# Optimization experiments

Hardware: AMD Instinct MI355X
Metric: run time of the kernel (lower is better)

The kernel has to match this reference:

```python
import jax, jax.numpy as jnp
import numpy as np

INPUT_DIMS = [300, 74, 35]
HIDDEN_DIMS = [512, 256, 256]
OUT_CELL = 256
OUT_DIM = 7
B, T = 128, 256


def setup_inputs() -> dict:
    key = jax.random.key(0)
    ks = jax.random.split(key, 32)
    inp = {}
    for i, d in enumerate(INPUT_DIMS):
        inp[f"x{i}"] = jax.random.normal(ks[i], (B, T, d), dtype=jnp.float32)
    ki = 3
    for i, (d, h) in enumerate(zip(INPUT_DIMS, HIDDEN_DIMS)):
        s_ih = 1.0 / np.sqrt(h)
        inp[f"W_ih{i}"] = jax.random.uniform(ks[ki + 0], (4 * h, d), jnp.float32, -s_ih, s_ih)
        inp[f"W_hh{i}"] = jax.random.uniform(ks[ki + 1], (4 * h, h), jnp.float32, -s_ih, s_ih)
        inp[f"b_ih{i}"] = jax.random.uniform(ks[ki + 2], (4 * h,), jnp.float32, -s_ih, s_ih)
        inp[f"b_hh{i}"] = jax.random.uniform(ks[ki + 3], (4 * h,), jnp.float32, -s_ih, s_ih)
        ki += 4
    H = sum(HIDDEN_DIMS)
    s1 = 1.0 / np.sqrt(H)
    s2 = 1.0 / np.sqrt(OUT_CELL)
    inp["fc_W1"] = jax.random.uniform(ks[ki + 0], (OUT_CELL, H), jnp.float32, -s1, s1)
    inp["fc_b1"] = jax.random.uniform(ks[ki + 1], (OUT_CELL,), jnp.float32, -s1, s1)
    inp["fc_W2"] = jax.random.uniform(ks[ki + 2], (OUT_DIM, OUT_CELL), jnp.float32, -s2, s2)
    inp["fc_b2"] = jax.random.uniform(ks[ki + 3], (OUT_DIM,), jnp.float32, -s2, s2)
    return inp


def _run_lstm(x, W_ih, W_hh, b_ih, b_hh):
    # x: [B, T, d] -> hidden trajectory [B, T, h]; PyTorch LSTMCell gate order i,f,g,o
    Bsz = x.shape[0]
    h4 = W_hh.shape[0]
    h = h4 // 4
    gx = jnp.einsum('btd,gd->btg', x, W_ih) + b_ih + b_hh  # precompute input contribution

    def step(carry, g_t):
        hp, cp = carry
        g = g_t + hp @ W_hh.T  # [B, 4h]
        i, f, gg, o = jnp.split(g, 4, axis=-1)
        c = jax.nn.sigmoid(f) * cp + jax.nn.sigmoid(i) * jnp.tanh(gg)
        hn = jax.nn.sigmoid(o) * jnp.tanh(c)
        return (hn, c), hn

    h0 = jnp.zeros((Bsz, h), x.dtype)
    c0 = jnp.zeros((Bsz, h), x.dtype)
    _, hs = jax.lax.scan(step, (h0, c0), gx.transpose(1, 0, 2))  # hs: [T, B, h]
    return hs.transpose(1, 0, 2)


def reference(x0, x1, x2,
              W_ih0, W_hh0, b_ih0, b_hh0,
              W_ih1, W_hh1, b_ih1, b_hh1,
              W_ih2, W_hh2, b_ih2, b_hh2,
              fc_W1, fc_b1, fc_W2, fc_b2):
    hs = [
        _run_lstm(x0, W_ih0, W_hh0, b_ih0, b_hh0),
        _run_lstm(x1, W_ih1, W_hh1, b_ih1, b_hh1),
        _run_lstm(x2, W_ih2, W_hh2, b_ih2, b_hh2),
    ]
    hcat = jnp.concatenate(hs, axis=-1)  # [B, T, sum(h)]
    # SimpleNet head (dropout identity at inference): Linear -> ReLU -> Linear
    z = jax.nn.relu(jnp.einsum('bth,ch->btc', hcat, fc_W1) + fc_b1)
    logits = jnp.einsum('btc,oc->bto', z, fc_W2) + fc_b2  # [B, T, out]
    return jax.nn.log_softmax(logits, axis=-1)
```

## Files before the change

kernel.cpp:

```cpp
#include <hip/hip_runtime.h>
#include <hip/hip_bf16.h>
#include <math.h>

typedef __hip_bfloat16 bf16;
typedef unsigned short ushort_t;
typedef unsigned long long ull_t;
typedef __attribute__((ext_vector_type(8))) short short8;
typedef __attribute__((ext_vector_type(4))) float f32x4;

constexpr int NB = 128;
constexpr int NT = 256;
constexpr int HCAT = 1024;
constexpr int KP0 = 320;
constexpr int KP1 = 128;
constexpr int KP2 = 64;

__device__ inline float bf2f(ushort_t u) {
  union { unsigned i; float f; } x; x.i = (unsigned)u << 16; return x.f;
}
__device__ inline ushort_t f2bf(float f) {
  bf16 b = __float2bfloat16(f);
  return *reinterpret_cast<ushort_t*>(&b);
}
__device__ inline float fsig(float x) {
  return __builtin_amdgcn_rcpf(1.f + __expf(-x));
}
__device__ inline float ftanh(float x) {
  return 2.f * __builtin_amdgcn_rcpf(1.f + __expf(-2.f * x)) - 1.f;
}

__global__ __launch_bounds__(256) void k_cvt_w(
    const float* __restrict__ in, ushort_t* __restrict__ out, int R, int K, int KP)
{
  int i = blockIdx.x * 256 + threadIdx.x;
  if (i >= R * KP) return;
  int r = i / KP, k = i - r * KP;
  out[i] = (k < K) ? f2bf(in[(size_t)r * K + k]) : (ushort_t)0;
}

__global__ __launch_bounds__(256) void k_cvt_x(
    const float* __restrict__ x, ushort_t* __restrict__ out,
    int d, int KP, int t0, int tcShift, int total)
{
  int i = blockIdx.x * 256 + threadIdx.x;
  if (i >= total) return;
  int row = i / KP, k = i - row * KP;
  int b = row >> tcShift, tl = row & ((1 << tcShift) - 1);
  out[i] = (k < d) ? f2bf(x[((size_t)b * NT + t0 + tl) * d + k]) : (ushort_t)0;
}

__global__ __launch_bounds__(256) void k_gemm(
    const ushort_t* __restrict__ A, const ushort_t* __restrict__ B, int KP,
    const float* __restrict__ bias0, const float* __restrict__ bias1,
    ushort_t* __restrict__ outb, float* __restrict__ outf, int ldc, int mode)
{
  __shared__ ushort_t As[2][64][72];
  __shared__ ushort_t Bs[2][64][72];
  const int row0 = blockIdx.x * 64;
  const int col0 = blockIdx.y * 64;
  const int tid  = threadIdx.x;
  const int lane = tid & 63;
  const int w    = tid >> 6;
  const int n    = lane & 15;
  const int quad = lane >> 4;
  const int sr = tid >> 2;
  const int sc = (tid & 3) * 16;

  const ushort_t* arow = A + (size_t)(row0 + sr) * KP + sc;
  const ushort_t* brow = B + (size_t)(col0 + sr) * KP + sc;

  short8 ra0 = *reinterpret_cast<const short8*>(arow);
  short8 ra1 = *reinterpret_cast<const short8*>(arow + 8);
  short8 rb0 = *reinterpret_cast<const short8*>(brow);
  short8 rb1 = *reinterpret_cast<const short8*>(brow + 8);
  *reinterpret_cast<short8*>(&As[0][sr][sc])     = ra0;
  *reinterpret_cast<short8*>(&As[0][sr][sc + 8]) = ra1;
  *reinterpret_cast<short8*>(&Bs[0][sr][sc])     = rb0;
  *reinterpret_cast<short8*>(&Bs[0][sr][sc + 8]) = rb1;

  f32x4 acc[4] = {{0,0,0,0},{0,0,0,0},{0,0,0,0},{0,0,0,0}};
  const int nch = KP >> 6;
  for (int ch = 0; ch < nch; ++ch) {
    __syncthreads();
    const int cur = ch & 1;
    if (ch + 1 < nch) {
      const ushort_t* an = arow + (ch + 1) * 64;
      const ushort_t* bn = brow + (ch + 1) * 64;
      ra0 = *reinterpret_cast<const short8*>(an);
      ra1 = *reinterpret_cast<const short8*>(an + 8);
      rb0 = *reinterpret_cast<const short8*>(bn);
      rb1 = *reinterpret_cast<const short8*>(bn + 8);
    }
#pragma unroll
    for (int kc = 0; kc < 2; ++kc) {
      short8 bfr = *reinterpret_cast<const short8*>(&Bs[cur][w * 16 + n][quad * 8 + kc * 32]);
#pragma unroll
      for (int mt = 0; mt < 4; ++mt) {
        short8 afr = *reinterpret_cast<const short8*>(&As[cur][mt * 16 + n][quad * 8 + kc * 32]);
        acc[mt] = __builtin_amdgcn_mfma_f32_16x16x32_bf16(afr, bfr, acc[mt], 0, 0, 0);
      }
    }
    if (ch + 1 < nch) {
      const int nxt = 1 - cur;
      *reinterpret_cast<short8*>(&As[nxt][sr][sc])     = ra0;
      *reinterpret_cast<short8*>(&As[nxt][sr][sc + 8]) = ra1;
      *reinterpret_cast<short8*>(&Bs[nxt][sr][sc])     = rb0;
      *reinterpret_cast<short8*>(&Bs[nxt][sr][sc + 8]) = rb1;
    }
  }

  const int col = col0 + w * 16 + n;
  if (mode == 0) {
    const float bsum = bias0[col] + bias1[col];
#pragma unroll
    for (int mt = 0; mt < 4; ++mt)
#pragma unroll
      for (int r = 0; r < 4; ++r) {
        int row = row0 + mt * 16 + quad * 4 + r;
        outb[(size_t)row * ldc + col] = f2bf(acc[mt][r] + bsum);
      }
  } else {
    const float bsum = bias0[col];
#pragma unroll
    for (int mt = 0; mt < 4; ++mt)
#pragma unroll
      for (int r = 0; r < 4; ++r) {
        int row = row0 + mt * 16 + quad * 4 + r;
        outf[(size_t)row * ldc + col] = fmaxf(acc[mt][r] + bsum, 0.f);
      }
  }
}

__global__ __launch_bounds__(256) void k_fc2(
    const float* __restrict__ Z, const float* __restrict__ W2,
    const float* __restrict__ b2, float* __restrict__ out, int t0, int tcShift)
{
  const int wave = threadIdx.x >> 6;
  const int lane = threadIdx.x & 63;
  const int bt = blockIdx.x * 4 + wave;
  const float* z = Z + (size_t)bt * 256;
  float zv[4];
#pragma unroll
  for (int j = 0; j < 4; ++j) zv[j] = z[lane + 64 * j];
  float lg[7];
#pragma unroll
  for (int o = 0; o < 7; ++o) {
    float a = 0.f;
#pragma unroll
    for (int j = 0; j < 4; ++j) a += zv[j] * W2[o * 256 + lane + 64 * j];
#pragma unroll
    for (int off = 32; off > 0; off >>= 1) a += __shfl_down(a, off, 64);
    lg[o] = a;
  }
  if (lane == 0) {
    const int b = bt >> tcShift;
    const int tl = bt & ((1 << tcShift) - 1);
    float* op = out + ((size_t)b * NT + t0 + tl) * 7;
    float lo[7];
    float m = -1e30f;
#pragma unroll
    for (int o = 0; o < 7; ++o) { lo[o] = lg[o] + b2[o]; m = fmaxf(m, lo[o]); }
    float s = 0.f;
#pragma unroll
    for (int o = 0; o < 7; ++o) s += expf(lo[o] - m);
    float lse = m + logf(s);
#pragma unroll
    for (int o = 0; o < 7; ++o) op[o] = lo[o] - lse;
  }
}

template<int HL>
__device__ void lstm_body(const float* __restrict__ Whh,
                          const ushort_t* __restrict__ gx,
                          unsigned* __restrict__ hb2,
                          float* __restrict__ cbuf,
                          ushort_t* __restrict__ hs,
                          ushort_t* htile,
                          float (*gbuf)[16][34],
                          int g, int u0, int hoff, int t0, int TC)
{
  constexpr int KC  = HL / 32;
  constexpr int LHP = HL + 8;
  constexpr int NGR = HL / 32;
  const int tid  = threadIdx.x;
  const int lane = tid & 63;
  const int wgate = tid >> 6;
  const int n    = lane & 15;
  const int quad = lane >> 4;

  short8 wfrag[2][KC];
#pragma unroll
  for (int tau = 0; tau < 2; ++tau) {
    const float* wrow = Whh + ((size_t)wgate * HL + u0 + 16 * tau + n) * HL + quad * 8;
#pragma unroll
    for (int kc = 0; kc < KC; ++kc) {
      short8 f;
#pragma unroll
      for (int j = 0; j < 8; ++j) f[j] = (short)f2bf(wrow[kc * 32 + j]);
      wfrag[tau][kc] = f;
    }
  }

  const int u  = tid & 31;
  const int bh = tid >> 5;
  const int bb0 = g * 16 + bh;
  const int bb1 = bb0 + 8;
  const int hcol = hoff + u0 + u;
  float c0 = cbuf[(size_t)bb0 * HCAT + hcol];
  float c1 = cbuf[(size_t)bb1 * HCAT + hcol];

  const int srow = wgate * 4 + (lane >> 4);
  const int scol = lane & 15;
  unsigned* htile32 = reinterpret_cast<unsigned*>(htile);

  const size_t G4 = (size_t)(4 * HL);
  float gxv0[4], gxv1[4];
#pragma unroll
  for (int q = 0; q < 4; ++q) {
    gxv0[q] = bf2f(gx[((size_t)bb0 * TC) * G4 + (size_t)q * HL + u0 + u]);
    gxv1[q] = bf2f(gx[((size_t)bb1 * TC) * G4 + (size_t)q * HL + u0 + u]);
  }

  const ull_t EPM = 0xFFFF0000FFFF0000ull;

  for (int t = 0; t < TC; ++t) {
    const unsigned ep = (unsigned)(t0 + t);
    const ull_t want = ((ull_t)ep << 16) | ((ull_t)ep << 48);
    const ull_t* src64 = reinterpret_cast<const ull_t*>(
        hb2 + ((size_t)(ep & 1) * NB + g * 16 + srow) * HCAT + hoff);

    ull_t vv[NGR];
    while (true) {
#pragma unroll
      for (int i = 0; i < NGR; ++i)
        vv[i] = __hip_atomic_load(src64 + scol + i * 16,
                                  __ATOMIC_RELAXED, __HIP_MEMORY_SCOPE_AGENT);
      ull_t bad = 0;
#pragma unroll
      for (int i = 0; i < NGR; ++i) bad |= (vv[i] ^ want) & EPM;
      if (bad == 0) break;
      __builtin_amdgcn_s_sleep(1);
    }
#pragma unroll
    for (int i = 0; i < NGR; ++i)
      htile32[srow * (LHP / 2) + scol + i * 16] =
          (unsigned)(vv[i] & 0xffffu) | ((unsigned)(vv[i] >> 16) & 0xffff0000u);
    __syncthreads();

    f32x4 acc0 = {0.f, 0.f, 0.f, 0.f};
    f32x4 acc1 = {0.f, 0.f, 0.f, 0.f};
#pragma unroll
    for (int kc = 0; kc < KC; ++kc) {
      short8 a = *reinterpret_cast<const short8*>(htile + n * LHP + quad * 8 + kc * 32);
      acc0 = __builtin_amdgcn_mfma_f32_16x16x32_bf16(a, wfrag[0][kc], acc0, 0, 0, 0);
      acc1 = __builtin_amdgcn_mfma_f32_16x16x32_bf16(a, wfrag[1][kc], acc1, 0, 0, 0);
    }
#pragma unroll
    for (int r = 0; r < 4; ++r) {
      gbuf[wgate][quad * 4 + r][n]      = acc0[r];
      gbuf[wgate][quad * 4 + r][16 + n] = acc1[r];
    }
    __syncthreads();

    float pi0 = gbuf[0][bh][u] + gxv0[0];
    float pf0 = gbuf[1][bh][u] + gxv0[1];
    float pg0 = gbuf[2][bh][u] + gxv0[2];
    float po0 = gbuf[3][bh][u] + gxv0[3];
    float pi1 = gbuf[0][bh + 8][u] + gxv1[0];
    float pf1 = gbuf[1][bh + 8][u] + gxv1[1];
    float pg1 = gbuf[2][bh + 8][u] + gxv1[2];
    float po1 = gbuf[3][bh + 8][u] + gxv1[3];

    float si0 = fsig(pi0), sf0 = fsig(pf0), so0 = fsig(po0);
    float tg0 = ftanh(pg0);
    c0 = sf0 * c0 + si0 * tg0;
    float h0 = so0 * ftanh(c0);
    float si1 = fsig(pi1), sf1 = fsig(pf1), so1 = fsig(po1);
    float tg1 = ftanh(pg1);
    c1 = sf1 * c1 + si1 * tg1;
    float h1 = so1 * ftanh(c1);

    const ushort_t hb0 = f2bf(h0), hb1 = f2bf(h1);
    const unsigned ep1 = (ep + 1) << 16;
    unsigned* nxt = hb2 + (size_t)((ep + 1) & 1) * NB * HCAT;
    __hip_atomic_store(nxt + (size_t)bb0 * HCAT + hcol, ep1 | (unsigned)hb0,
                       __ATOMIC_RELAXED, __HIP_MEMORY_SCOPE_AGENT);
    __hip_atomic_store(nxt + (size_t)bb1 * HCAT + hcol, ep1 | (unsigned)hb1,
                       __ATOMIC_RELAXED, __HIP_MEMORY_SCOPE_AGENT);

    hs[((size_t)bb0 * TC + t) * HCAT + hcol] = hb0;
    hs[((size_t)bb1 * TC + t) * HCAT + hcol] = hb1;
    if (t + 1 < TC) {
#pragma unroll
      for (int q = 0; q < 4; ++q) {
        gxv0[q] = bf2f(gx[((size_t)bb0 * TC + t + 1) * G4 + (size_t)q * HL + u0 + u]);
        gxv1[q] = bf2f(gx[((size_t)bb1 * TC + t + 1) * G4 + (size_t)q * HL + u0 + u]);
      }
    }
  }
  cbuf[(size_t)bb0 * HCAT + hcol] = c0;
  cbuf[(size_t)bb1 * HCAT + hcol] = c1;
}

__global__ __launch_bounds__(256, 1) void k_lstm(
    const float* __restrict__ Whh0, const float* __restrict__ Whh1,
    const float* __restrict__ Whh2,
    const ushort_t* __restrict__ gx0, const ushort_t* __restrict__ gx1,
    const ushort_t* __restrict__ gx2,
    unsigned* __restrict__ hb2, float* __restrict__ cbuf,
    ushort_t* __restrict__ hs,
    int t0, int TC)
{
  __shared__ ushort_t htile[16 * 520];
  __shared__ float gbuf[4][16][34];
  const int g    = blockIdx.x & 7;
  const int rank = blockIdx.x >> 3;
  if (rank < 16) {
    lstm_body<512>(Whh0, gx0, hb2, cbuf, hs, htile, gbuf,
                   g, rank * 32, 0, t0, TC);
  } else if (rank < 24) {
    lstm_body<256>(Whh1, gx1, hb2, cbuf, hs, htile, gbuf,
                   g, (rank - 16) * 32, 512, t0, TC);
  } else {
    lstm_body<256>(Whh2, gx2, hb2, cbuf, hs, htile, gbuf,
                   g, (rank - 24) * 32, 768, t0, TC);
  }
}

__global__ void k_fill(float* __restrict__ out, int n, float v) {
  int i = blockIdx.x * 256 + threadIdx.x;
  if (i < n) out[i] = v;
}

extern "C" void kernel_launch(void* const* d_in, const int* in_sizes, int n_in,
                              void* d_out, int out_size, void* d_ws, size_t ws_size,
                              hipStream_t stream) {
  (void)in_sizes; (void)n_in;
  const float* x0  = (const float*)d_in[0];
  const float* x1  = (const float*)d_in[1];
  const float* x2  = (const float*)d_in[2];
  const float* Wih0 = (const float*)d_in[3];
  const float* Whh0 = (const float*)d_in[4];
  const float* bih0 = (const float*)d_in[5];
  const float* bhh0 = (const float*)d_in[6];
  const float* Wih1 = (const float*)d_in[7];
  const float* Whh1 = (const float*)d_in[8];
  const float* bih1 = (const float*)d_in[9];
  const float* bhh1 = (const float*)d_in[10];
  const float* Wih2 = (const float*)d_in[11];
  const float* Whh2 = (const float*)d_in[12];
  const float* bih2 = (const float*)d_in[13];
  const float* bhh2 = (const float*)d_in[14];
  const float* W1 = (const float*)d_in[15];
  const float* b1 = (const float*)d_in[16];
  const float* W2 = (const float*)d_in[17];
  const float* b2 = (const float*)d_in[18];
  float* out = (float*)d_out;

  const size_t szHbuf  = (size_t)2 * NB * HCAT * 4;
  const size_t szCbuf  = (size_t)NB * HCAT * 4;
  const size_t szWb0   = (size_t)2048 * KP0 * 2;
  const size_t szWb1   = (size_t)1024 * KP1 * 2;
  const size_t szWb2   = (size_t)1024 * KP2 * 2;
  const size_t szW1b   = (size_t)256 * 1024 * 2;

  const int cands[6] = {256, 128, 64, 32, 16, 8};
  int TC = 0;
  for (int ci = 0; ci < 6; ++ci) {
    int tc = cands[ci];
    size_t rows = (size_t)NB * tc;
    size_t o = 0;
    auto al = [&](size_t bytes) { o += (bytes + 255) & ~(size_t)255; };
    al(szHbuf); al(szCbuf);
    al(szWb0); al(szWb1); al(szWb2); al(szW1b);
    al(rows * HCAT * 2);
    al(rows * 256 * 4);
    al(rows * 2048 * 2);
    al(rows * 1024 * 2);
    al(rows * 1024 * 2);
    al(rows * KP0 * 2);
    al(rows * KP1 * 2);
    al(rows * KP2 * 2);
    if (o <= ws_size) { TC = tc; break; }
  }
  if (TC == 0) {
    k_fill<<<dim3((out_size + 255) / 256), dim3(256), 0, stream>>>(out, out_size, -8888.f);
    return;
  }
  const int tcShift = __builtin_ctz(TC);
  const size_t rows = (size_t)NB * TC;

  char* ws = (char*)d_ws;
  size_t off = 0;
  auto alloc = [&](size_t bytes) -> void* {
    void* p = ws + off;
    off += (bytes + 255) & ~(size_t)255;
    return p;
  };
  unsigned* hb2  = (unsigned*)alloc(szHbuf);
  float* cbuf    = (float*)alloc(szCbuf);
  size_t staticEnd = off;
  ushort_t* wb0  = (ushort_t*)alloc(szWb0);
  ushort_t* wb1  = (ushort_t*)alloc(szWb1);
  ushort_t* wb2  = (ushort_t*)alloc(szWb2);
  ushort_t* w1b  = (ushort_t*)alloc(szW1b);
  ushort_t* hs   = (ushort_t*)alloc(rows * HCAT * 2);
  float* z       = (float*)alloc(rows * 256 * 4);
  ushort_t* gx0  = (ushort_t*)alloc(rows * 2048 * 2);
  ushort_t* gx1  = (ushort_t*)alloc(rows * 1024 * 2);
  ushort_t* gx2  = (ushort_t*)alloc(rows * 1024 * 2);
  ushort_t* xb0  = (ushort_t*)alloc(rows * KP0 * 2);
  ushort_t* xb1  = (ushort_t*)alloc(rows * KP1 * 2);
  ushort_t* xb2  = (ushort_t*)alloc(rows * KP2 * 2);

  hipMemsetAsync(ws, 0, staticEnd, stream);

  dim3 blk(256);
  k_cvt_w<<<dim3((2048 * KP0 + 255) / 256), blk, 0, stream>>>(Wih0, wb0, 2048, 300, KP0);
  k_cvt_w<<<dim3((1024 * KP1 + 255) / 256), blk, 0, stream>>>(Wih1, wb1, 1024, 74, KP1);
  k_cvt_w<<<dim3((1024 * KP2 + 255) / 256), blk, 0, stream>>>(Wih2, wb2, 1024, 35, KP2);
  k_cvt_w<<<dim3((256 * 1024 + 255) / 256), blk, 0, stream>>>(W1, w1b, 256, 1024, 1024);

  const int rb = (int)(rows / 64);
  for (int t0 = 0; t0 < NT; t0 += TC) {
    int tot0 = (int)(rows * KP0), tot1 = (int)(rows * KP1), tot2 = (int)(rows * KP2);
    k_cvt_x<<<dim3((tot0 + 255) / 256), blk, 0, stream>>>(x0, xb0, 300, KP0, t0, tcShift, tot0);
    k_cvt_x<<<dim3((tot1 + 255) / 256), blk, 0, stream>>>(x1, xb1, 74, KP1, t0, tcShift, tot1);
    k_cvt_x<<<dim3((tot2 + 255) / 256), blk, 0, stream>>>(x2, xb2, 35, KP2, t0, tcShift, tot2);

    k_gemm<<<dim3(rb, 2048 / 64), blk, 0, stream>>>(xb0, wb0, KP0, bih0, bhh0, gx0, nullptr, 2048, 0);
    k_gemm<<<dim3(rb, 1024 / 64), blk, 0, stream>>>(xb1, wb1, KP1, bih1, bhh1, gx1, nullptr, 1024, 0);
    k_gemm<<<dim3(rb, 1024 / 64), blk, 0, stream>>>(xb2, wb2, KP2, bih2, bhh2, gx2, nullptr, 1024, 0);

    k_lstm<<<dim3(256), blk, 0, stream>>>(Whh0, Whh1, Whh2,
                                          gx0, gx1, gx2,
                                          hb2, cbuf, hs, t0, TC);

    k_gemm<<<dim3(rb, 256 / 64), blk, 0, stream>>>(hs, w1b, 1024, b1, nullptr, nullptr, z, 256, 1);
    k_fc2<<<dim3((int)(rows / 4)), blk, 0, stream>>>(z, W2, b2, out, t0, tcShift);
  }
}
```

Measured before the change: 919.9 us.

## Enlarge GEMM tiles to 128x128 and prefetch next-step hidden state in LSTM

The bf16 MFMA GEMM now uses 128x128 output tiles with a 2x2 wave layout, each wave computing 4x4 fragments. This raises data reuse per LDS load and cuts the number of blocks. In the recurrent LSTM kernel, the spin-wait now issues the atomic loads for the next timestep's hidden state right after storing the current one, so the first poll's latency overlaps the hs writes and gx loads. The risks are fewer blocks for the smaller GEMMs, higher register and LDS use, and possibly more stale first polls.

```diff
diff --git a/kernel.cpp b/kernel.cpp
--- a/kernel.cpp
+++ b/kernel.cpp
@@ -54,31 +54,36 @@
     const float* __restrict__ bias0, const float* __restrict__ bias1,
     ushort_t* __restrict__ outb, float* __restrict__ outf, int ldc, int mode)
 {
-  __shared__ ushort_t As[2][64][72];
-  __shared__ ushort_t Bs[2][64][72];
-  const int row0 = blockIdx.x * 64;
-  const int col0 = blockIdx.y * 64;
+  __shared__ ushort_t As[2][128][72];
+  __shared__ ushort_t Bs[2][128][72];
+  const int row0 = blockIdx.x * 128;
+  const int col0 = blockIdx.y * 128;
   const int tid  = threadIdx.x;
   const int lane = tid & 63;
   const int w    = tid >> 6;
+  const int wr   = w >> 1;
+  const int wc   = w & 1;
   const int n    = lane & 15;
   const int quad = lane >> 4;
-  const int sr = tid >> 2;
-  const int sc = (tid & 3) * 16;
+  const int sr = tid >> 1;
+  const int sc = (tid & 1) * 32;
 
   const ushort_t* arow = A + (size_t)(row0 + sr) * KP + sc;
   const ushort_t* brow = B + (size_t)(col0 + sr) * KP + sc;
 
-  short8 ra0 = *reinterpret_cast<const short8*>(arow);
-  short8 ra1 = *reinterpret_cast<const short8*>(arow + 8);
-  short8 rb0 = *reinterpret_cast<const short8*>(brow);
-  short8 rb1 = *reinterpret_cast<const short8*>(brow + 8);
-  *reinterpret_cast<short8*>(&As[0][sr][sc])     = ra0;
-  *reinterpret_cast<short8*>(&As[0][sr][sc + 8]) = ra1;
-  *reinterpret_cast<short8*>(&Bs[0][sr][sc])     = rb0;
-  *reinterpret_cast<short8*>(&Bs[0][sr][sc + 8]) = rb1;
-
-  f32x4 acc[4] = {{0,0,0,0},{0,0,0,0},{0,0,0,0},{0,0,0,0}};
+  short8 ra[4], rb[4];
+#pragma unroll
+  for (int j = 0; j < 4; ++j) {
+    ra[j] = *reinterpret_cast<const short8*>(arow + j * 8);
+    rb[j] = *reinterpret_cast<const short8*>(brow + j * 8);
+  }
+#pragma unroll
+  for (int j = 0; j < 4; ++j) {
+    *reinterpret_cast<short8*>(&As[0][sr][sc + j * 8]) = ra[j];
+    *reinterpret_cast<short8*>(&Bs[0][sr][sc + j * 8]) = rb[j];
+  }
+
+  f32x4 acc[4][4] = {};
   const int nch = KP >> 6;
   for (int ch = 0; ch < nch; ++ch) {
     __syncthreads();
@@ -86,48 +91,60 @@
     if (ch + 1 < nch) {
       const ushort_t* an = arow + (ch + 1) * 64;
       const ushort_t* bn = brow + (ch + 1) * 64;
-      ra0 = *reinterpret_cast<const short8*>(an);
-      ra1 = *reinterpret_cast<const short8*>(an + 8);
-      rb0 = *reinterpret_cast<const short8*>(bn);
-      rb1 = *reinterpret_cast<const short8*>(bn + 8);
+#pragma unroll
+      for (int j = 0; j < 4; ++j) {
+        ra[j] = *reinterpret_cast<const short8*>(an + j * 8);
+        rb[j] = *reinterpret_cast<const short8*>(bn + j * 8);
+      }
     }
 #pragma unroll
     for (int kc = 0; kc < 2; ++kc) {
-      short8 bfr = *reinterpret_cast<const short8*>(&Bs[cur][w * 16 + n][quad * 8 + kc * 32]);
+      short8 bfr[4];
+#pragma unroll
+      for (int nt = 0; nt < 4; ++nt)
+        bfr[nt] = *reinterpret_cast<const short8*>(
+            &Bs[cur][wc * 64 + nt * 16 + n][quad * 8 + kc * 32]);
 #pragma unroll
       for (int mt = 0; mt < 4; ++mt) {
-        short8 afr = *reinterpret_cast<const short8*>(&As[cur][mt * 16 + n][quad * 8 + kc * 32]);
-        acc[mt] = __builtin_amdgcn_mfma_f32_16x16x32_bf16(afr, bfr, acc[mt], 0, 0, 0);
+        short8 afr = *reinterpret_cast<const short8*>(
+            &As[cur][wr * 64 + mt * 16 + n][quad * 8 + kc * 32]);
+#pragma unroll
+        for (int nt = 0; nt < 4; ++nt)
+          acc[mt][nt] = __builtin_amdgcn_mfma_f32_16x16x32_bf16(afr, bfr[nt], acc[mt][nt], 0, 0, 0);
       }
     }
     if (ch + 1 < nch) {
       const int nxt = 1 - cur;
-      *reinterpret_cast<short8*>(&As[nxt][sr][sc])     = ra0;
-      *reinterpret_cast<short8*>(&As[nxt][sr][sc + 8]) = ra1;
-      *reinterpret_cast<short8*>(&Bs[nxt][sr][sc])     = rb0;
-      *reinterpret_cast<short8*>(&Bs[nxt][sr][sc + 8]) = rb1;
-    }
-  }
-
-  const int col = col0 + w * 16 + n;
-  if (mode == 0) {
-    const float bsum = bias0[col] + bias1[col];
-#pragma unroll
-    for (int mt = 0; mt < 4; ++mt)
-#pragma unroll
-      for (int r = 0; r < 4; ++r) {
-        int row = row0 + mt * 16 + quad * 4 + r;
-        outb[(size_t)row * ldc + col] = f2bf(acc[mt][r] + bsum);
+#pragma unroll
+      for (int j = 0; j < 4; ++j) {
+        *reinterpret_cast<short8*>(&As[nxt][sr][sc + j * 8]) = ra[j];
+        *reinterpret_cast<short8*>(&Bs[nxt][sr][sc + j * 8]) = rb[j];
       }
-  } else {
-    const float bsum = bias0[col];
-#pragma unroll
-    for (int mt = 0; mt < 4; ++mt)
-#pragma unroll
-      for (int r = 0; r < 4; ++r) {
-        int row = row0 + mt * 16 + quad * 4 + r;
-        outf[(size_t)row * ldc + col] = fmaxf(acc[mt][r] + bsum, 0.f);
-      }
+    }
+  }
+
+#pragma unroll
+  for (int nt = 0; nt < 4; ++nt) {
+    const int col = col0 + wc * 64 + nt * 16 + n;
+    if (mode == 0) {
+      const float bsum = bias0[col] + bias1[col];
+#pragma unroll
+      for (int mt = 0; mt < 4; ++mt)
+#pragma unroll
+        for (int r = 0; r < 4; ++r) {
+          int row = row0 + wr * 64 + mt * 16 + quad * 4 + r;
+          outb[(size_t)row * ldc + col] = f2bf(acc[mt][nt][r] + bsum);
+        }
+    } else {
+      const float bsum = bias0[col];
+#pragma unroll
+      for (int mt = 0; mt < 4; ++mt)
+#pragma unroll
+        for (int r = 0; r < 4; ++r) {
+          int row = row0 + wr * 64 + mt * 16 + quad * 4 + r;
+          outf[(size_t)row * ldc + col] = fmaxf(acc[mt][nt][r] + bsum, 0.f);
+        }
+    }
   }
 }
 
@@ -223,23 +240,32 @@
 
   const ull_t EPM = 0xFFFF0000FFFF0000ull;
 
+  ull_t vv[NGR];
+  {
+    const ull_t* src64 = reinterpret_cast<const ull_t*>(
+        hb2 + ((size_t)((unsigned)t0 & 1) * NB + g * 16 + srow) * HCAT + hoff);
+#pragma unroll
+    for (int i = 0; i < NGR; ++i)
+      vv[i] = __hip_atomic_load(src64 + scol + i * 16,
+                                __ATOMIC_RELAXED, __HIP_MEMORY_SCOPE_AGENT);
+  }
+
   for (int t = 0; t < TC; ++t) {
     const unsigned ep = (unsigned)(t0 + t);
     const ull_t want = ((ull_t)ep << 16) | ((ull_t)ep << 48);
     const ull_t* src64 = reinterpret_cast<const ull_t*>(
         hb2 + ((size_t)(ep & 1) * NB + g * 16 + srow) * HCAT + hoff);
 
-    ull_t vv[NGR];
     while (true) {
+      ull_t bad = 0;
+#pragma unroll
+      for (int i = 0; i < NGR; ++i) bad |= (vv[i] ^ want) & EPM;
+      if (bad == 0) break;
+      __builtin_amdgcn_s_sleep(1);
 #pragma unroll
       for (int i = 0; i < NGR; ++i)
         vv[i] = __hip_atomic_load(src64 + scol + i * 16,
                                   __ATOMIC_RELAXED, __HIP_MEMORY_SCOPE_AGENT);
-      ull_t bad = 0;
-#pragma unroll
-      for (int i = 0; i < NGR; ++i) bad |= (vv[i] ^ want) & EPM;
-      if (bad == 0) break;
-      __builtin_amdgcn_s_sleep(1);
     }
 #pragma unroll
     for (int i = 0; i < NGR; ++i)
@@ -287,6 +313,15 @@
                        __ATOMIC_RELAXED, __HIP_MEMORY_SCOPE_AGENT);
     __hip_atomic_store(nxt + (size_t)bb1 * HCAT + hcol, ep1 | (unsigned)hb1,
                        __ATOMIC_RELAXED, __HIP_MEMORY_SCOPE_AGENT);
+
+    if (t + 1 < TC) {
+      const ull_t* nsrc = reinterpret_cast<const ull_t*>(
+          hb2 + ((size_t)((ep + 1) & 1) * NB + g * 16 + srow) * HCAT + hoff);
+#pragma unroll
+      for (int i = 0; i < NGR; ++i)
+        vv[i] = __hip_atomic_load(nsrc + scol + i * 16,
+                                  __ATOMIC_RELAXED, __HIP_MEMORY_SCOPE_AGENT);
+    }
 
     hs[((size_t)bb0 * TC + t) * HCAT + hcol] = hb0;
     hs[((size_t)bb1 * TC + t) * HCAT + hcol] = hb1;
@@ -421,22 +456,22 @@
   k_cvt_w<<<dim3((1024 * KP2 + 255) / 256), blk, 0, stream>>>(Wih2, wb2, 1024, 35, KP2);
   k_cvt_w<<<dim3((256 * 1024 + 255) / 256), blk, 0, stream>>>(W1, w1b, 256, 1024, 1024);
 
-  const int rb = (int)(rows / 64);
+  const int rbm = (int)(rows / 128);
   for (int t0 = 0; t0 < NT; t0 += TC) {
     int tot0 = (int)(rows * KP0), tot1 = (int)(rows * KP1), tot2 = (int)(rows * KP2);
     k_cvt_x<<<dim3((tot0 + 255) / 256), blk, 0, stream>>>(x0, xb0, 300, KP0, t0, tcShift, tot0);
     k_cvt_x<<<dim3((tot1 + 255) / 256), blk, 0, stream>>>(x1, xb1, 74, KP1, t0, tcShift, tot1);
     k_cvt_x<<<dim3((tot2 + 255) / 256), blk, 0, stream>>>(x2, xb2, 35, KP2, t0, tcShift, tot2);
 
-    k_gemm<<<dim3(rb, 2048 / 64), blk, 0, stream>>>(xb0, wb0, KP0, bih0, bhh0, gx0, nullptr, 2048, 0);
-    k_gemm<<<dim3(rb, 1024 / 64), blk, 0, stream>>>(xb1, wb1, KP1, bih1, bhh1, gx1, nullptr, 1024, 0);
-    k_gemm<<<dim3(rb, 1024 / 64), blk, 0, stream>>>(xb2, wb2, KP2, bih2, bhh2, gx2, nullptr, 1024, 0);
+    k_gemm<<<dim3(rbm, 2048 / 128), blk, 0, stream>>>(xb0, wb0, KP0, bih0, bhh0, gx0, nullptr, 2048, 0);
+    k_gemm<<<dim3(rbm, 1024 / 128), blk, 0, stream>>>(xb1, wb1, KP1, bih1, bhh1, gx1, nullptr, 1024, 0);
+    k_gemm<<<dim3(rbm, 1024 / 128), blk, 0, stream>>>(xb2, wb2, KP2, bih2, bhh2, gx2, nullptr, 1024, 0);
 
     k_lstm<<<dim3(256), blk, 0, stream>>>(Whh0, Whh1, Whh2,
                                           gx0, gx1, gx2,
                                           hb2, cbuf, hs, t0, TC);
 
-    k_gemm<<<dim3(rb, 256 / 64), blk, 0, stream>>>(hs, w1b, 1024, b1, nullptr, nullptr, z, 256, 1);
+    k_gemm<<<dim3(rbm, 256 / 128), blk, 0, stream>>>(hs, w1b, 1024, b1, nullptr, nullptr, z, 256, 1);
     k_fc2<<<dim3((int)(rows / 4)), blk, 0, stream>>>(z, W2, b2, out, t0, tcShift);
   }
 }
```

New measurement: 1.218 ms. 1.32x slower.

## Fuse LSTM input projection into the recurrent kernel, overlapped with the h-wait

Applied to the files above, without the earlier changes.

Drops the separate x conversion kernels and the three input-projection GEMMs. Each LSTM block now keeps its slice of W_ih as bf16 MFMA fragments in registers and stages the next timestep's x row into a double-buffered shared tile. It runs the x·W_ih MFMAs while it is still polling for the previous hidden state, and folds the biases in directly. This removes the gx round trips through memory and several launches, at the cost of more registers, more shared memory, and extra per-step work inside the latency-critical recurrence.

```diff
diff --git a/kernel.cpp b/kernel.cpp
--- a/kernel.cpp
+++ b/kernel.cpp
@@ -36,17 +36,6 @@
   if (i >= R * KP) return;
   int r = i / KP, k = i - r * KP;
   out[i] = (k < K) ? f2bf(in[(size_t)r * K + k]) : (ushort_t)0;
-}
-
-__global__ __launch_bounds__(256) void k_cvt_x(
-    const float* __restrict__ x, ushort_t* __restrict__ out,
-    int d, int KP, int t0, int tcShift, int total)
-{
-  int i = blockIdx.x * 256 + threadIdx.x;
-  if (i >= total) return;
-  int row = i / KP, k = i - row * KP;
-  int b = row >> tcShift, tl = row & ((1 << tcShift) - 1);
-  out[i] = (k < d) ? f2bf(x[((size_t)b * NT + t0 + tl) * d + k]) : (ushort_t)0;
 }
 
 __global__ __launch_bounds__(256) void k_gemm(
@@ -169,19 +158,26 @@
   }
 }
 
-template<int HL>
+template<int HL, int KP, int D>
 __device__ void lstm_body(const float* __restrict__ Whh,
-                          const ushort_t* __restrict__ gx,
+                          const float* __restrict__ Wih,
+                          const float* __restrict__ bih,
+                          const float* __restrict__ bhh,
+                          const float* __restrict__ x,
                           unsigned* __restrict__ hb2,
                           float* __restrict__ cbuf,
                           ushort_t* __restrict__ hs,
                           ushort_t* htile,
                           float (*gbuf)[16][34],
+                          ushort_t* xtile,
                           int g, int u0, int hoff, int t0, int TC)
 {
   constexpr int KC  = HL / 32;
+  constexpr int KCX = KP / 32;
   constexpr int LHP = HL + 8;
+  constexpr int XLP = KP + 8;
   constexpr int NGR = HL / 32;
+  constexpr int CPT = KP / 16;
   const int tid  = threadIdx.x;
   const int lane = tid & 63;
   const int wgate = tid >> 6;
@@ -198,6 +194,21 @@
 #pragma unroll
       for (int j = 0; j < 8; ++j) f[j] = (short)f2bf(wrow[kc * 32 + j]);
       wfrag[tau][kc] = f;
+    }
+  }
+  short8 wifrag[2][KCX];
+#pragma unroll
+  for (int tau = 0; tau < 2; ++tau) {
+    const float* wrow = Wih + ((size_t)wgate * HL + u0 + 16 * tau + n) * D;
+#pragma unroll
+    for (int kc = 0; kc < KCX; ++kc) {
+      short8 f;
+#pragma unroll
+      for (int j = 0; j < 8; ++j) {
+        int k = kc * 32 + quad * 8 + j;
+        f[j] = (k < D) ? (short)f2bf(wrow[k]) : (short)0;
+      }
+      wifrag[tau][kc] = f;
     }
   }
 
@@ -208,18 +219,27 @@
   const int hcol = hoff + u0 + u;
   float c0 = cbuf[(size_t)bb0 * HCAT + hcol];
   float c1 = cbuf[(size_t)bb1 * HCAT + hcol];
+  float bs[4];
+#pragma unroll
+  for (int q = 0; q < 4; ++q)
+    bs[q] = bih[q * HL + u0 + u] + bhh[q * HL + u0 + u];
 
   const int srow = wgate * 4 + (lane >> 4);
   const int scol = lane & 15;
   unsigned* htile32 = reinterpret_cast<unsigned*>(htile);
 
-  const size_t G4 = (size_t)(4 * HL);
-  float gxv0[4], gxv1[4];
-#pragma unroll
-  for (int q = 0; q < 4; ++q) {
-    gxv0[q] = bf2f(gx[((size_t)bb0 * TC) * G4 + (size_t)q * HL + u0 + u]);
-    gxv1[q] = bf2f(gx[((size_t)bb1 * TC) * G4 + (size_t)q * HL + u0 + u]);
-  }
+  const int xr = tid >> 4, xc = tid & 15;
+
+  {
+    const float* xrow = x + ((size_t)(g * 16 + xr) * NT + t0) * D;
+    ushort_t* dst = xtile + ((size_t)(t0 & 1) * 16 + xr) * XLP + xc * CPT;
+#pragma unroll
+    for (int j = 0; j < CPT; ++j) {
+      int k = xc * CPT + j;
+      dst[j] = (k < D) ? f2bf(xrow[k]) : (ushort_t)0;
+    }
+  }
+  __syncthreads();
 
   const ull_t EPM = 0xFFFF0000FFFF0000ull;
 
@@ -230,16 +250,34 @@
         hb2 + ((size_t)(ep & 1) * NB + g * 16 + srow) * HCAT + hoff);
 
     ull_t vv[NGR];
+#pragma unroll
+    for (int i = 0; i < NGR; ++i)
+      vv[i] = __hip_atomic_load(src64 + scol + i * 16,
+                                __ATOMIC_RELAXED, __HIP_MEMORY_SCOPE_AGENT);
+
+    f32x4 acc0 = {0.f, 0.f, 0.f, 0.f};
+    f32x4 acc1 = {0.f, 0.f, 0.f, 0.f};
+    {
+      const ushort_t* xt = xtile + (size_t)(ep & 1) * 16 * XLP;
+#pragma unroll
+      for (int kc = 0; kc < KCX; ++kc) {
+        short8 a = *reinterpret_cast<const short8*>(xt + n * XLP + quad * 8 + kc * 32);
+        acc0 = __builtin_amdgcn_mfma_f32_16x16x32_bf16(a, wifrag[0][kc], acc0, 0, 0, 0);
+        acc1 = __builtin_amdgcn_mfma_f32_16x16x32_bf16(a, wifrag[1][kc], acc1, 0, 0, 0);
+      }
+    }
+    __builtin_amdgcn_sched_barrier(0);
+
     while (true) {
+      ull_t bad = 0;
+#pragma unroll
+      for (int i = 0; i < NGR; ++i) bad |= (vv[i] ^ want) & EPM;
+      if (bad == 0) break;
+      __builtin_amdgcn_s_sleep(1);
 #pragma unroll
       for (int i = 0; i < NGR; ++i)
         vv[i] = __hip_atomic_load(src64 + scol + i * 16,
                                   __ATOMIC_RELAXED, __HIP_MEMORY_SCOPE_AGENT);
-      ull_t bad = 0;
-#pragma unroll
-      for (int i = 0; i < NGR; ++i) bad |= (vv[i] ^ want) & EPM;
-      if (bad == 0) break;
-      __builtin_amdgcn_s_sleep(1);
     }
 #pragma unroll
     for (int i = 0; i < NGR; ++i)
@@ -247,8 +285,17 @@
           (unsigned)(vv[i] & 0xffffu) | ((unsigned)(vv[i] >> 16) & 0xffff0000u);
     __syncthreads();
 
-    f32x4 acc0 = {0.f, 0.f, 0.f, 0.f};
-    f32x4 acc1 = {0.f, 0.f, 0.f, 0.f};
+    const bool doX = (t + 1 < TC);
+    float xv[CPT];
+    if (doX) {
+      const float* xrow1 = x + ((size_t)(g * 16 + xr) * NT + t0 + t + 1) * D;
+#pragma unroll
+      for (int j = 0; j < CPT; ++j) {
+        int k = xc * CPT + j;
+        xv[j] = (k < D) ? xrow1[k] : 0.f;
+      }
+    }
+
 #pragma unroll
     for (int kc = 0; kc < KC; ++kc) {
       short8 a = *reinterpret_cast<const short8*>(htile + n * LHP + quad * 8 + kc * 32);
@@ -260,16 +307,22 @@
       gbuf[wgate][quad * 4 + r][n]      = acc0[r];
       gbuf[wgate][quad * 4 + r][16 + n] = acc1[r];
     }
+
+    if (doX) {
+      ushort_t* dst = xtile + ((size_t)((ep + 1) & 1) * 16 + xr) * XLP + xc * CPT;
+#pragma unroll
+      for (int j = 0; j < CPT; ++j) dst[j] = f2bf(xv[j]);
+    }
     __syncthreads();
 
-    float pi0 = gbuf[0][bh][u] + gxv0[0];
-    float pf0 = gbuf[1][bh][u] + gxv0[1];
-    float pg0 = gbuf[2][bh][u] + gxv0[2];
-    float po0 = gbuf[3][bh][u] + gxv0[3];
-    float pi1 = gbuf[0][bh + 8][u] + gxv1[0];
-    float pf1 = gbuf[1][bh + 8][u] + gxv1[1];
-    float pg1 = gbuf[2][bh + 8][u] + gxv1[2];
-    float po1 = gbuf[3][bh + 8][u] + gxv1[3];
+    float pi0 = gbuf[0][bh][u] + bs[0];
+    float pf0 = gbuf[1][bh][u] + bs[1];
+    float pg0 = gbuf[2][bh][u] + bs[2];
+    float po0 = gbuf[3][bh][u] + bs[3];
+    float pi1 = gbuf[0][bh + 8][u] + bs[0];
+    float pf1 = gbuf[1][bh + 8][u] + bs[1];
+    float pg1 = gbuf[2][bh + 8][u] + bs[2];
+    float po1 = gbuf[3][bh + 8][u] + bs[3];
 
     float si0 = fsig(pi0), sf0 = fsig(pf0), so0 = fsig(po0);
     float tg0 = ftanh(pg0);
@@ -290,13 +343,6 @@
 
     hs[((size_t)bb0 * TC + t) * HCAT + hcol] = hb0;
     hs[((size_t)bb1 * TC + t) * HCAT + hcol] = hb1;
-    if (t + 1 < TC) {
-#pragma unroll
-      for (int q = 0; q < 4; ++q) {
-        gxv0[q] = bf2f(gx[((size_t)bb0 * TC + t + 1) * G4 + (size_t)q * HL + u0 + u]);
-        gxv1[q] = bf2f(gx[((size_t)bb1 * TC + t + 1) * G4 + (size_t)q * HL + u0 + u]);
-      }
-    }
   }
   cbuf[(size_t)bb0 * HCAT + hcol] = c0;
   cbuf[(size_t)bb1 * HCAT + hcol] = c1;
@@ -305,25 +351,32 @@
 __global__ __launch_bounds__(256, 1) void k_lstm(
     const float* __restrict__ Whh0, const float* __restrict__ Whh1,
     const float* __restrict__ Whh2,
-    const ushort_t* __restrict__ gx0, const ushort_t* __restrict__ gx1,
-    const ushort_t* __restrict__ gx2,
+    const float* __restrict__ Wih0, const float* __restrict__ Wih1,
+    const float* __restrict__ Wih2,
+    const float* __restrict__ bih0, const float* __restrict__ bih1,
+    const float* __restrict__ bih2,
+    const float* __restrict__ bhh0, const float* __restrict__ bhh1,
+    const float* __restrict__ bhh2,
+    const float* __restrict__ x0, const float* __restrict__ x1,
+    const float* __restrict__ x2,
     unsigned* __restrict__ hb2, float* __restrict__ cbuf,
     ushort_t* __restrict__ hs,
     int t0, int TC)
 {
   __shared__ ushort_t htile[16 * 520];
   __shared__ float gbuf[4][16][34];
+  __shared__ ushort_t xtile[2 * 16 * 328];
   const int g    = blockIdx.x & 7;
   const int rank = blockIdx.x >> 3;
   if (rank < 16) {
-    lstm_body<512>(Whh0, gx0, hb2, cbuf, hs, htile, gbuf,
-                   g, rank * 32, 0, t0, TC);
+    lstm_body<512, KP0, 300>(Whh0, Wih0, bih0, bhh0, x0, hb2, cbuf, hs,
+                             htile, gbuf, xtile, g, rank * 32, 0, t0, TC);
   } else if (rank < 24) {
-    lstm_body<256>(Whh1, gx1, hb2, cbuf, hs, htile, gbuf,
-                   g, (rank - 16) * 32, 512, t0, TC);
+    lstm_body<256, KP1, 74>(Whh1, Wih1, bih1, bhh1, x1, hb2, cbuf, hs,
+                            htile, gbuf, xtile, g, (rank - 16) * 32, 512, t0, TC);
   } else {
-    lstm_body<256>(Whh2, gx2, hb2, cbuf, hs, htile, gbuf,
-                   g, (rank - 24) * 32, 768, t0, TC);
+    lstm_body<256, KP2, 35>(Whh2, Wih2, bih2, bhh2, x2, hb2, cbuf, hs,
+                            htile, gbuf, xtile, g, (rank - 24) * 32, 768, t0, TC);
   }
 }
 
@@ -359,9 +412,6 @@
 
   const size_t szHbuf  = (size_t)2 * NB * HCAT * 4;
   const size_t szCbuf  = (size_t)NB * HCAT * 4;
-  const size_t szWb0   = (size_t)2048 * KP0 * 2;
-  const size_t szWb1   = (size_t)1024 * KP1 * 2;
-  const size_t szWb2   = (size_t)1024 * KP2 * 2;
   const size_t szW1b   = (size_t)256 * 1024 * 2;
 
   const int cands[6] = {256, 128, 64, 32, 16, 8};
@@ -371,16 +421,9 @@
     size_t rows = (size_t)NB * tc;
     size_t o = 0;
     auto al = [&](size_t bytes) { o += (bytes + 255) & ~(size_t)255; };
-    al(szHbuf); al(szCbuf);
-    al(szWb0); al(szWb1); al(szWb2); al(szW1b);
+    al(szHbuf); al(szCbuf); al(szW1b);
     al(rows * HCAT * 2);
     al(rows * 256 * 4);
-    al(rows * 2048 * 2);
-    al(rows * 1024 * 2);
-    al(rows * 1024 * 2);
-    al(rows * KP0 * 2);
-    al(rows * KP1 * 2);
-    al(rows * KP2 * 2);
     if (o <= ws_size) { TC = tc; break; }
   }
   if (TC == 0) {
@@ -400,40 +443,22 @@
   unsigned* hb2  = (unsigned*)alloc(szHbuf);
   float* cbuf    = (float*)alloc(szCbuf);
   size_t staticEnd = off;
-  ushort_t* wb0  = (ushort_t*)alloc(szWb0);
-  ushort_t* wb1  = (ushort_t*)alloc(szWb1);
-  ushort_t* wb2  = (ushort_t*)alloc(szWb2);
   ushort_t* w1b  = (ushort_t*)alloc(szW1b);
   ushort_t* hs   = (ushort_t*)alloc(rows * HCAT * 2);
   float* z       = (float*)alloc(rows * 256 * 4);
-  ushort_t* gx0  = (ushort_t*)alloc(rows * 2048 * 2);
-  ushort_t* gx1  = (ushort_t*)alloc(rows * 1024 * 2);
-  ushort_t* gx2  = (ushort_t*)alloc(rows * 1024 * 2);
-  ushort_t* xb0  = (ushort_t*)alloc(rows * KP0 * 2);
-  ushort_t* xb1  = (ushort_t*)alloc(rows * KP1 * 2);
-  ushort_t* xb2  = (ushort_t*)alloc(rows * KP2 * 2);
 
   hipMemsetAsync(ws, 0, staticEnd, stream);
 
   dim3 blk(256);
-  k_cvt_w<<<dim3((2048 * KP0 + 255) / 256), blk, 0, stream>>>(Wih0, wb0, 2048, 300, KP0);
-  k_cvt_w<<<dim3((1024 * KP1 + 255) / 256), blk, 0, stream>>>(Wih1, wb1, 1024, 74, KP1);
-  k_cvt_w<<<dim3((1024 * KP2 + 255) / 256), blk, 0, stream>>>(Wih2, wb2, 1024, 35, KP2);
   k_cvt_w<<<dim3((256 * 1024 + 255) / 256), blk, 0, stream>>>(W1, w1b, 256, 1024, 1024);
 
   const int rb = (int)(rows / 64);
   for (int t0 = 0; t0 < NT; t0 += TC) {
-    int tot0 = (int)(rows * KP0), tot1 = (int)(rows * KP1), tot2 = (int)(rows * KP2);
-    k_cvt_x<<<dim3((tot0 + 255) / 256), blk, 0, stream>>>(x0, xb0, 300, KP0, t0, tcShift, tot0);
-    k_cvt_x<<<dim3((tot1 + 255) / 256), blk, 0, stream>>>(x1, xb1, 74, KP1, t0, tcShift, tot1);
-    k_cvt_x<<<dim3((tot2 + 255) / 256), blk, 0, stream>>>(x2, xb2, 35, KP2, t0, tcShift, tot2);
-
-    k_gemm<<<dim3(rb, 2048 / 64), blk, 0, stream>>>(xb0, wb0, KP0, bih0, bhh0, gx0, nullptr, 2048, 0);
-    k_gemm<<<dim3(rb, 1024 / 64), blk, 0, stream>>>(xb1, wb1, KP1, bih1, bhh1, gx1, nullptr, 1024, 0);
-    k_gemm<<<dim3(rb, 1024 / 64), blk, 0, stream>>>(xb2, wb2, KP2, bih2, bhh2, gx2, nullptr, 1024, 0);
-
     k_lstm<<<dim3(256), blk, 0, stream>>>(Whh0, Whh1, Whh2,
-                                          gx0, gx1, gx2,
+                                          Wih0, Wih1, Wih2,
+                                          bih0, bih1, bih2,
+                                          bhh0, bhh1, bhh2,
+                                          x0, x1, x2,
                                           hb2, cbuf, hs, t0, TC);
 
     k_gemm<<<dim3(rb, 256 / 64), blk, 0, stream>>>(hs, w1b, 1024, b1, nullptr, nullptr, z, 256, 1);
```

Result: slower. 1.234 ms (+34.1%).
